# Optimization experiments

Measured on AMD Instinct MI355X. Metric: run time of the kernel, lower is better.

## Reference

```python
import jax, jax.numpy as jnp
import numpy as np

# --- static config (matches init_kwargs) ---
B, S, DIM = 1, 2048, 1024
H, G, DK, DV = 16, 4, 64, 64
HPG = H // G
L, D, LSEL, NSEL, W = 32, 16, 64, 16, 512
NCMP = (S - L) // D + 1            # number of compressed blocks over full prefill
J = S // LSEL                      # number of selection blocks
GH = 32                            # gate hidden
NEG = -1e30


def rope(x, pos):
    # x: [B, S, N, Dh]; llama-style half rotation
    Dh = x.shape[-1]
    inv = 1.0 / (10000.0 ** (np.arange(0, Dh, 2) / Dh))
    ang = pos[:, None] * inv[None, :]                      # [S, Dh/2]
    cos = jnp.asarray(np.cos(ang), jnp.float32)[None, :, None, :]
    sin = jnp.asarray(np.sin(ang), jnp.float32)[None, :, None, :]
    x1, x2 = jnp.split(x, 2, axis=-1)
    return jnp.concatenate([x1 * cos - x2 * sin, x2 * cos + x1 * sin], axis=-1)


def masked_softmax(s, m):
    p = jax.nn.softmax(jnp.where(m, s, NEG), axis=-1)
    # rows with no visible keys produce 0 output (empty attention)
    return jnp.where(jnp.any(m, axis=-1, keepdims=True), p, 0.0)


def setup_inputs() -> dict:
    key = jax.random.key(0)
    ks = jax.random.split(key, 12)
    def w(k, shape, fan):
        return jax.random.normal(k, shape, jnp.float32) / np.sqrt(fan)
    return {
        'x': jax.random.normal(ks[0], (B, S, DIM), jnp.float32),
        'W_Q': w(ks[1], (DIM, H * DK), DIM),
        'W_K_sel': w(ks[2], (DIM, G * DK), DIM),
        'W_V_sel': w(ks[3], (DIM, G * DV), DIM),
        'W_K_win': w(ks[4], (DIM, G * DK), DIM),
        'W_V_win': w(ks[5], (DIM, G * DV), DIM),
        'W_K_cmp': w(ks[6], (DIM, G * DK), DIM),
        'W_V_cmp': w(ks[7], (DIM, G * DV), DIM),
        'W_out': w(ks[8], (H * DV, DIM), H * DV),
        'gate_w1': w(ks[9], (DK, GH), DK),
        'gate_b1': jnp.zeros((GH,), jnp.float32),
        'gate_w2': 0.1 * jax.random.normal(ks[10], (GH, 3), jnp.float32),
        'gate_b2': jnp.zeros((3,), jnp.float32),
    }


def reference(x, W_Q, W_K_sel, W_V_sel, W_K_win, W_V_win, W_K_cmp, W_V_cmp,
              W_out, gate_w1, gate_b1, gate_w2, gate_b2):
    pos = np.arange(S)
    s_ = np.arange(S)
    scale = 1.0 / np.sqrt(DK)

    Q = rope((x @ W_Q).reshape(B, S, H, DK), pos).reshape(B, S, G, HPG, DK)

    def proj_kv(Wk, Wv):
        K = rope((x @ Wk).reshape(B, S, G, DK), pos).transpose(0, 2, 1, 3)  # [B,G,S,Dk]
        V = (x @ Wv).reshape(B, S, G, DV).transpose(0, 2, 1, 3)            # [B,G,S,Dv]
        return K, V

    K_sel, V_sel = proj_kv(W_K_sel, W_V_sel)
    K_win, V_win = proj_kv(W_K_win, W_V_win)
    K_cr, V_cr = proj_kv(W_K_cmp, W_V_cmp)

    # --- compressed branch: avg-pool (len L, stride D) of roped K / raw V ---
    bidx = np.arange(NCMP)[:, None] * D + np.arange(L)[None, :]   # [NCMP, L]
    K_cmp = K_cr[:, :, bidx].mean(axis=3)                         # [B,G,NCMP,Dk]
    V_cmp = V_cr[:, :, bidx].mean(axis=3)
    vis_c = (np.arange(NCMP)[None, :] * D + L) <= (s_[:, None] + 1)  # block fully in past
    sc_c = jnp.einsum('bsghd,bgcd->bsghc', Q, K_cmp) * scale
    p_cmp = masked_softmax(sc_c, jnp.asarray(vis_c)[None, :, None, None, :])
    O_cmp = jnp.einsum('bsghc,bgce->bsghe', p_cmp, V_cmp)

    # --- map compressed probs -> selection-block scores (overlap fractions) ---
    i0 = np.arange(NCMP)[:, None] * D
    j0 = np.arange(J)[None, :] * LSEL
    ov = np.maximum(0, np.minimum(i0 + L, j0 + LSEL) - np.maximum(i0, j0)) / L
    p_grp = jnp.einsum('bsghc,cj->bsgj', p_cmp, jnp.asarray(ov, np.float32))  # sum over heads in group

    vis_j = (np.arange(J)[None, :] * LSEL) <= s_[:, None]
    forced = (np.arange(J)[None, :] == 0) | (np.arange(J)[None, :] == (s_ // LSEL)[:, None])
    score = jnp.where(jnp.asarray(vis_j)[None, :, None, :], p_grp, NEG)
    score = jnp.where(jnp.asarray(forced)[None, :, None, :], 1e9, score)  # force block 0 + current block
    topj = jax.lax.top_k(score, NSEL)[1]                                   # [B,S,G,NSEL]
    blk = jax.nn.one_hot(topj, J, dtype=jnp.float32).sum(axis=-2) > 0      # [B,S,G,J]

    tok2blk = np.repeat(np.arange(J), LSEL)[:S]
    causal = s_[:, None] >= s_[None, :]                                    # u <= t
    sel_mask = blk[:, :, :, tok2blk] & jnp.asarray(causal)[None, :, None, :]  # [B,S,G,S]
    sc_s = jnp.einsum('bsghd,bgud->bsghu', Q, K_sel) * scale
    O_sel = jnp.einsum('bsghu,bgue->bsghe',
                       masked_softmax(sc_s, sel_mask[:, :, :, None, :]), V_sel)

    # --- sliding window branch ---
    win_mask = causal & (s_[None, :] > s_[:, None] - W)
    sc_w = jnp.einsum('bsghd,bgud->bsghu', Q, K_win) * scale
    O_win = jnp.einsum('bsghu,bgue->bsghe',
                       masked_softmax(sc_w, jnp.asarray(win_mask)[None, :, None, None, :]), V_win)

    # --- gating MLP on head-pooled query per group ---
    gl = jax.nn.silu(Q.mean(axis=3) @ gate_w1 + gate_b1) @ gate_w2 + gate_b2  # [B,S,G,3]
    pg = jax.nn.softmax(gl, axis=-1)
    t2 = jax.lax.top_k(gl, 2)[0]
    peaked = (t2[..., 0] - t2[..., 1]) > 50.0
    gates = jnp.where(peaked[..., None],
                      jax.nn.one_hot(jnp.argmax(gl, axis=-1), 3, dtype=gl.dtype), pg)

    O = (gates[..., 0, None, None] * O_cmp
         + gates[..., 1, None, None] * O_sel
         + gates[..., 2, None, None] * O_win)          # [B,S,G,h,Dv]
    return O.reshape(B, S, H * DV) @ W_out
```

## Files before the change

kernel.cpp:

```cpp
#include <hip/hip_runtime.h>
#include <math.h>

#define S 2048
#define DIM 1024
#define H 16
#define G 4
#define HPG 4
#define DK 64
#define DV 64
#define NCMP 127
#define JBLK 32
#define NSEL 16
#define WWIN 512
#define GH 32
#define SCL2 0.18033688011112042f

typedef __attribute__((ext_vector_type(8))) __bf16 bf16x8;
typedef __attribute__((ext_vector_type(4))) float f32x4;

__device__ __forceinline__ unsigned short f2bf(float f) {
  unsigned u = __float_as_uint(f);
  unsigned r = (u + 0x7FFFu + ((u >> 16) & 1u)) >> 16;
  return (unsigned short)r;
}

__device__ __forceinline__ unsigned short f2bf_hw(float f) {
  __bf16 b = (__bf16)f;
  return *(unsigned short*)&b;
}

__device__ __forceinline__ f32x4 mfma16(bf16x8 a, bf16x8 b, f32x4 c) {
  return __builtin_amdgcn_mfma_f32_16x16x32_bf16(a, b, c, 0, 0, 0);
}

__global__ void rope_table(float* __restrict__ cosT, float* __restrict__ sinT) {
  int idx = blockIdx.x * blockDim.x + threadIdx.x;
  if (idx >= S * 32) return;
  int s = idx >> 5, i = idx & 31;
  double inv = pow(10000.0, -2.0 * (double)i / 64.0);
  double ang = (double)s * inv;
  cosT[idx] = (float)cos(ang);
  sinT[idx] = (float)sin(ang);
}

__device__ __forceinline__ void gemm_body(const float* __restrict__ A,
                                          const float* __restrict__ B,
                                          float* __restrict__ C,
                                          int N, int K, int bm, int bn,
                                          float* As , float* Bs ) {
  int tid = threadIdx.x;
  int tr = tid >> 4, tc = tid & 15;
  float acc[4][4] = {{0.f}};
  int arow = tid >> 2;
  int kba = (tid & 3) << 3;
  int brow = tid >> 4;
  int bcol = (tid & 15) << 2;
  const float* Ab = A + (size_t)(bm * 64) * K;
  const float* Bb = B + bn * 64;

  float4 a0 = *(const float4*)(Ab + (size_t)arow * K + kba);
  float4 a1 = *(const float4*)(Ab + (size_t)arow * K + kba + 4);
  float4 b0 = *(const float4*)(Bb + (size_t)brow * N + bcol);
  float4 b1 = *(const float4*)(Bb + (size_t)(brow + 16) * N + bcol);

  for (int k0 = 0; k0 < K; k0 += 32) {
    __syncthreads();
    {
      float av[8] = {a0.x, a0.y, a0.z, a0.w, a1.x, a1.y, a1.z, a1.w};
#pragma unroll
      for (int i = 0; i < 8; ++i) {
        int k = kba + i;
        As[k * 64 + (arow ^ (((k >> 3) & 3) << 3))] = av[i];
      }
      *(float4*)&Bs[brow * 64 + bcol] = b0;
      *(float4*)&Bs[(brow + 16) * 64 + bcol] = b1;
    }
    __syncthreads();
    if (k0 + 32 < K) {
      a0 = *(const float4*)(Ab + (size_t)arow * K + k0 + 32 + kba);
      a1 = *(const float4*)(Ab + (size_t)arow * K + k0 + 32 + kba + 4);
      b0 = *(const float4*)(Bb + (size_t)(k0 + 32 + brow) * N + bcol);
      b1 = *(const float4*)(Bb + (size_t)(k0 + 32 + brow + 16) * N + bcol);
    }
#pragma unroll
    for (int kk = 0; kk < 32; ++kk) {
      float4 a = *(const float4*)&As[kk * 64 + ((tr << 2) ^ (((kk >> 3) & 3) << 3))];
      float4 b = *(const float4*)&Bs[kk * 64 + (tc << 2)];
      acc[0][0] += a.x * b.x; acc[0][1] += a.x * b.y; acc[0][2] += a.x * b.z; acc[0][3] += a.x * b.w;
      acc[1][0] += a.y * b.x; acc[1][1] += a.y * b.y; acc[1][2] += a.y * b.z; acc[1][3] += a.y * b.w;
      acc[2][0] += a.z * b.x; acc[2][1] += a.z * b.y; acc[2][2] += a.z * b.z; acc[2][3] += a.z * b.w;
      acc[3][0] += a.w * b.x; acc[3][1] += a.w * b.y; acc[3][2] += a.w * b.z; acc[3][3] += a.w * b.w;
    }
  }
  for (int i = 0; i < 4; ++i)
    for (int jj = 0; jj < 4; ++jj)
      C[(size_t)(bm * 64 + (tr << 2) + i) * N + bn * 64 + (tc << 2) + jj] = acc[i][jj];
}

__global__ __launch_bounds__(256) void gemm_f32(const float* __restrict__ A,
                                                const float* __restrict__ B,
                                                float* __restrict__ C,
                                                int N, int K) {
  __shared__ float As[32 * 64];
  __shared__ float Bs[32 * 64];
  gemm_body(A, B, C, N, K, blockIdx.y, blockIdx.x, As, Bs);
}

__global__ __launch_bounds__(256) void gemm_kv2(const float* __restrict__ x,
                                                const float* __restrict__ W0,
                                                const float* __restrict__ W1,
                                                float* __restrict__ out) {
  __shared__ float As[32 * 64];
  __shared__ float Bs[32 * 64];
  const float* B = blockIdx.z ? W1 : W0;
  gemm_body(x, B, out + (size_t)blockIdx.z * S * 256, 256, DIM, blockIdx.y,
            blockIdx.x, As, Bs);
}

__global__ void rope_apply(float* __restrict__ a, const float* __restrict__ cosT,
                           const float* __restrict__ sinT, int NH, int total) {
  int idx = blockIdx.x * blockDim.x + threadIdx.x;
  if (idx >= total) return;
  int i = idx & 31;
  int rest = idx >> 5;
  int n = rest % NH;
  int s = rest / NH;
  float c = cosT[s * 32 + i], sn = sinT[s * 32 + i];
  float* base = a + (size_t)(s * NH + n) * 64;
  float x1 = base[i], x2 = base[i + 32];
  base[i] = x1 * c - x2 * sn;
  base[i + 32] = x2 * c + x1 * sn;
}

__global__ __launch_bounds__(256) void fconv(const float* __restrict__ a,
                                             unsigned short* __restrict__ b) {
  int idx = (blockIdx.x * 256 + threadIdx.x) * 8;
  float4 x = *(const float4*)&a[idx];
  float4 y = *(const float4*)&a[idx + 4];
  union { unsigned short us[8]; float4 f4; } t;
  t.us[0] = f2bf(x.x); t.us[1] = f2bf(x.y); t.us[2] = f2bf(x.z); t.us[3] = f2bf(x.w);
  t.us[4] = f2bf(y.x); t.us[5] = f2bf(y.y); t.us[6] = f2bf(y.z); t.us[7] = f2bf(y.w);
  *(float4*)&b[idx] = t.f4;
}

__global__ __launch_bounds__(256) void wtrans(const float* __restrict__ W0,
                                              const float* __restrict__ W1,
                                              const float* __restrict__ W2,
                                              const float* __restrict__ W3,
                                              unsigned short* __restrict__ Wt) {
  __shared__ float t[64][65];
  int k0 = blockIdx.x * 64;
  int n0 = blockIdx.y * 64;
  int m = blockIdx.z;
  const float* W = (m == 0) ? W0 : (m == 1) ? W1 : (m == 2) ? W2 : W3;
  int tid = threadIdx.x;
  int rr = tid >> 4, c4 = (tid & 15) * 4;
#pragma unroll
  for (int e = 0; e < 4; ++e) {
    int row = rr + e * 16;
    float4 v = *(const float4*)(W + (size_t)(k0 + row) * 256 + n0 + c4);
    t[c4 + 0][row] = v.x;
    t[c4 + 1][row] = v.y;
    t[c4 + 2][row] = v.z;
    t[c4 + 3][row] = v.w;
  }
  __syncthreads();
#pragma unroll
  for (int e = 0; e < 2; ++e) {
    int flat = tid + e * 256;
    int col = flat >> 3, kc = (flat & 7) * 8;
    union { unsigned short us[8]; float4 f4; } u;
#pragma unroll
    for (int i = 0; i < 8; ++i) u.us[i] = f2bf(t[col][kc + i]);
    *(float4*)(Wt + ((size_t)m * 256 + n0 + col) * 1024 + k0 + kc) = u.f4;
  }
}

__global__ __launch_bounds__(256) void wtrans_o(const float* __restrict__ W,
                                                unsigned short* __restrict__ Wt) {
  __shared__ float t[64][65];
  int k0 = blockIdx.x * 64;
  int n0 = blockIdx.y * 64;
  int tid = threadIdx.x;
  int rr = tid >> 4, c4 = (tid & 15) * 4;
#pragma unroll
  for (int e = 0; e < 4; ++e) {
    int row = rr + e * 16;
    float4 v = *(const float4*)(W + (size_t)(k0 + row) * 1024 + n0 + c4);
    t[c4 + 0][row] = v.x;
    t[c4 + 1][row] = v.y;
    t[c4 + 2][row] = v.z;
    t[c4 + 3][row] = v.w;
  }
  __syncthreads();
#pragma unroll
  for (int e = 0; e < 2; ++e) {
    int flat = tid + e * 256;
    int col = flat >> 3, kc = (flat & 7) * 8;
    union { unsigned short us[8]; float4 f4; } u;
#pragma unroll
    for (int i = 0; i < 8; ++i) u.us[i] = f2bf(t[col][kc + i]);
    *(float4*)(Wt + (size_t)(n0 + col) * 1024 + k0 + kc) = u.f4;
  }
}

__global__ __launch_bounds__(256) void proj_bf16(
    const unsigned short* __restrict__ xb, const unsigned short* __restrict__ Wt,
    const float* __restrict__ cosT, const float* __restrict__ sinT,
    unsigned short* __restrict__ Kb_s, unsigned short* __restrict__ Vt_s,
    unsigned short* __restrict__ Kb_w, unsigned short* __restrict__ Vt_w) {
  __shared__ unsigned short xs[64 * 64];
  __shared__ unsigned short ws[64 * 64];
  int s0 = blockIdx.x * 64;
  int g = blockIdx.y;
  int mat = blockIdx.z;
  int tid = threadIdx.x, w = tid >> 6, lane = tid & 63;
  int l15 = lane & 15, lg = lane >> 4;
  int rswz = (l15 & 7) << 3;
  bool isV = (mat & 1);
  const unsigned short* wt = Wt + ((size_t)mat * 256 + g * 64) * 1024;

  f32x4 acc[4];
#pragma unroll
  for (int nt = 0; nt < 4; ++nt) acc[nt] = (f32x4){0.f, 0.f, 0.f, 0.f};

  for (int k0 = 0; k0 < DIM; k0 += 64) {
#pragma unroll
    for (int e = 0; e < 2; ++e) {
      int flat = tid + e * 256;
      int row = flat >> 3, cc = flat & 7;
      int dsti = row * 64 + ((cc ^ (row & 7)) << 3);
      *(float4*)&xs[dsti] = *(const float4*)(xb + (size_t)(s0 + row) * DIM + k0 + cc * 8);
      *(float4*)&ws[dsti] = *(const float4*)(wt + (size_t)row * DIM + k0 + cc * 8);
    }
    __syncthreads();
    const unsigned short* aP = isV ? ws : xs;
    const unsigned short* bP = isV ? xs : ws;
    int arow = w * 16 + l15;
    bf16x8 af[2];
#pragma unroll
    for (int kc = 0; kc < 2; ++kc)
      af[kc] = *(const bf16x8*)&aP[(arow * 64 + kc * 32 + lg * 8) ^ rswz];
#pragma unroll
    for (int nt = 0; nt < 4; ++nt) {
      int brow = nt * 16 + l15;
      bf16x8 b0 = *(const bf16x8*)&bP[(brow * 64 + lg * 8) ^ rswz];
      bf16x8 b1 = *(const bf16x8*)&bP[(brow * 64 + 32 + lg * 8) ^ rswz];
      acc[nt] = mfma16(af[0], b0, acc[nt]);
      acc[nt] = mfma16(af[1], b1, acc[nt]);
    }
    __syncthreads();
  }

  if (!isV) {
    unsigned short* Kb = (mat == 0) ? Kb_s : Kb_w;
#pragma unroll
    for (int rr = 0; rr < 4; ++rr) {
      int tok = s0 + w * 16 + lg * 4 + rr;
#pragma unroll
      for (int p = 0; p < 2; ++p) {
        int i = p * 16 + l15;
        float c = cosT[tok * 32 + i], sn = sinT[tok * 32 + i];
        float x1 = acc[p][rr], x2 = acc[p + 2][rr];
        Kb[((size_t)g * S + tok) * 64 + i] = f2bf(x1 * c - x2 * sn);
        Kb[((size_t)g * S + tok) * 64 + i + 32] = f2bf(x2 * c + x1 * sn);
      }
    }
  } else {
    unsigned short* Vt = (mat == 1) ? Vt_s : Vt_w;
#pragma unroll
    for (int rr = 0; rr < 4; ++rr) {
      int col = w * 16 + lg * 4 + rr;
#pragma unroll
      for (int nt = 0; nt < 4; ++nt) {
        int tok = s0 + nt * 16 + l15;
        Vt[((size_t)g * 64 + col) * S + tok] = f2bf(acc[nt][rr]);
      }
    }
  }
}

__global__ __launch_bounds__(256) void gemm_out(const unsigned short* __restrict__ Ob,
                                                const unsigned short* __restrict__ Wt,
                                                float* __restrict__ out) {
  __shared__ unsigned short xs[64 * 64];
  __shared__ unsigned short ws[64 * 64];
  int s0 = blockIdx.x * 64;
  int n0 = blockIdx.y * 64;
  int tid = threadIdx.x, w = tid >> 6, lane = tid & 63;
  int l15 = lane & 15, lg = lane >> 4;
  int rswz = (l15 & 7) << 3;

  f32x4 acc[4];
#pragma unroll
  for (int nt = 0; nt < 4; ++nt) acc[nt] = (f32x4){0.f, 0.f, 0.f, 0.f};

  for (int k0 = 0; k0 < DIM; k0 += 64) {
#pragma unroll
    for (int e = 0; e < 2; ++e) {
      int flat = tid + e * 256;
      int row = flat >> 3, cc = flat & 7;
      int dsti = row * 64 + ((cc ^ (row & 7)) << 3);
      *(float4*)&xs[dsti] = *(const float4*)(Ob + (size_t)(s0 + row) * DIM + k0 + cc * 8);
      *(float4*)&ws[dsti] = *(const float4*)(Wt + (size_t)(n0 + row) * DIM + k0 + cc * 8);
    }
    __syncthreads();
    int arow = w * 16 + l15;
    bf16x8 af0 = *(const bf16x8*)&xs[(arow * 64 + lg * 8) ^ rswz];
    bf16x8 af1 = *(const bf16x8*)&xs[(arow * 64 + 32 + lg * 8) ^ rswz];
#pragma unroll
    for (int nt = 0; nt < 4; ++nt) {
      int brow = nt * 16 + l15;
      bf16x8 b0 = *(const bf16x8*)&ws[(brow * 64 + lg * 8) ^ rswz];
      bf16x8 b1 = *(const bf16x8*)&ws[(brow * 64 + 32 + lg * 8) ^ rswz];
      acc[nt] = mfma16(af0, b0, acc[nt]);
      acc[nt] = mfma16(af1, b1, acc[nt]);
    }
    __syncthreads();
  }

#pragma unroll
  for (int nt = 0; nt < 4; ++nt)
#pragma unroll
    for (int rr = 0; rr < 4; ++rr)
      out[(size_t)(s0 + w * 16 + lg * 4 + rr) * 1024 + n0 + nt * 16 + l15] =
          acc[nt][rr];
}

__global__ void pool_cmp(const float* __restrict__ Kcr, const float* __restrict__ Vcr,
                         float* __restrict__ Kc, float* __restrict__ Vc) {
  int c = blockIdx.x, g = blockIdx.y, d = threadIdx.x;
  float sk = 0.f, sv = 0.f;
  for (int l = 0; l < 32; ++l) {
    int t = c * 16 + l;
    sk += Kcr[(size_t)(t * G + g) * 64 + d];
    sv += Vcr[(size_t)(t * G + g) * 64 + d];
  }
  Kc[(size_t)(g * NCMP + c) * 64 + d] = sk * (1.f / 32.f);
  Vc[(size_t)(g * NCMP + c) * 64 + d] = sv * (1.f / 32.f);
}

__global__ __launch_bounds__(256) void cmp_attn(const float* __restrict__ Q,
                                                const float* __restrict__ Kc,
                                                const float* __restrict__ Vc,
                                                float* __restrict__ Ocmp,
                                                unsigned int* __restrict__ selm) {
  int s = blockIdx.x, g = blockIdx.y;
  __shared__ float q4[4][64];
  __shared__ float sc[4][128];
  __shared__ float pg[JBLK];
  int tid = threadIdx.x;
  int nvis = (s >= 31) ? (((s - 31) >> 4) + 1) : 0;
  {
    int h = tid >> 6, d = tid & 63;
    q4[h][d] = Q[(size_t)(s * H + g * HPG + h) * 64 + d];
  }
  __syncthreads();

  if (tid < 128) {
    int c = tid;
    if (c < nvis) {
      float a0 = 0.f, a1 = 0.f, a2 = 0.f, a3 = 0.f;
      const float* kr = &Kc[(size_t)(g * NCMP + c) * 64];
#pragma unroll 4
      for (int kk = 0; kk < 16; ++kk) {
        float4 kv = *(const float4*)&kr[kk * 4];
        float4 q0 = *(const float4*)&q4[0][kk * 4];
        float4 q1 = *(const float4*)&q4[1][kk * 4];
        float4 q2 = *(const float4*)&q4[2][kk * 4];
        float4 q3 = *(const float4*)&q4[3][kk * 4];
        a0 += q0.x * kv.x + q0.y * kv.y + q0.z * kv.z + q0.w * kv.w;
        a1 += q1.x * kv.x + q1.y * kv.y + q1.z * kv.z + q1.w * kv.w;
        a2 += q2.x * kv.x + q2.y * kv.y + q2.z * kv.z + q2.w * kv.w;
        a3 += q3.x * kv.x + q3.y * kv.y + q3.z * kv.z + q3.w * kv.w;
      }
      sc[0][c] = a0 * 0.125f;
      sc[1][c] = a1 * 0.125f;
      sc[2][c] = a2 * 0.125f;
      sc[3][c] = a3 * 0.125f;
    } else {
      sc[0][c] = -INFINITY;
      sc[1][c] = -INFINITY;
      sc[2][c] = -INFINITY;
      sc[3][c] = -INFINITY;
    }
  }
  __syncthreads();

  int w = tid >> 6, lane = tid & 63;
  {
    float v0 = sc[w][lane];
    float v1 = (lane + 64 < NCMP) ? sc[w][lane + 64] : -INFINITY;
    float m = fmaxf(v0, v1);
    for (int off = 32; off; off >>= 1) m = fmaxf(m, __shfl_xor(m, off));
    float e0 = (m > -INFINITY && v0 > -INFINITY) ? expf(v0 - m) : 0.f;
    float e1 = (m > -INFINITY && v1 > -INFINITY) ? expf(v1 - m) : 0.f;
    float sum = e0 + e1;
    for (int off = 32; off; off >>= 1) sum += __shfl_xor(sum, off);
    float inv = (sum > 0.f) ? 1.f / sum : 0.f;
    sc[w][lane] = e0 * inv;
    if (lane + 64 < NCMP) sc[w][lane + 64] = e1 * inv;
    if (lane == 63) sc[w][127] = 0.f;
  }
  __syncthreads();

  {
    int h = tid >> 6, d = tid & 63;
    float o = 0.f;
#pragma unroll 4
    for (int c = 0; c < nvis; ++c) o += sc[h][c] * Vc[(size_t)(g * NCMP + c) * 64 + d];
    Ocmp[(size_t)(s * H + g * HPG + h) * 64 + d] = o;
  }

  if (tid < JBLK) {
    int j = tid;
    float a = 0.f;
#pragma unroll
    for (int h = 0; h < 4; ++h) {
      const float* row = sc[h];
      float v = row[4 * j] + row[4 * j + 1] + row[4 * j + 2] + 0.5f * row[4 * j + 3];
      if (j > 0) v += 0.5f * row[4 * j - 1];
      a += v;
    }
    pg[j] = a;
  }
  __syncthreads();

  if (tid < 64) {
    int j = tid & 31;
    int cur = s >> 6;
    float v = (j * 64 <= s) ? pg[j] : -1e30f;
    if (j == 0 || j == cur) v = 1e9f;
    unsigned int mask = 0;
#pragma unroll 1
    for (int n = 0; n < NSEL; ++n) {
      float bv = v;
      int bj = j;
#pragma unroll
      for (int off = 1; off < 32; off <<= 1) {
        float ov = __shfl_xor(bv, off);
        int oj = __shfl_xor(bj, off);
        if (ov > bv || (ov == bv && oj < bj)) { bv = ov; bj = oj; }
      }
      mask |= 1u << bj;
      if (j == bj) v = -INFINITY;
    }
    if (tid == 0) selm[(size_t)s * G + g] = mask;
  }
}

__global__ __launch_bounds__(256) void attn_fused(
    const unsigned short* __restrict__ Qbf,
    const unsigned short* __restrict__ Kbs, const unsigned short* __restrict__ Vts,
    const unsigned short* __restrict__ Kbw, const unsigned short* __restrict__ Vtw,
    const unsigned int* __restrict__ selm,
    float* __restrict__ Osel, float* __restrict__ Owin) {
  __shared__ unsigned short Kl[64 * 64];
  __shared__ unsigned short Vt[64 * 64];
  __shared__ unsigned short Pl[4][16 * 64];
  __shared__ unsigned int sel_l[16];
  __shared__ int blist[JBLK];
  __shared__ int nB_s;

  int t0 = blockIdx.x * 16;
  int g = blockIdx.y;
  int mode = blockIdx.z;
  int tid = threadIdx.x;
  int w = tid >> 6, lane = tid & 63;
  int l15 = lane & 15, lg = lane >> 4;
  int rswz = (l15 & 7) << 3;
  int jdiag = t0 >> 6;

  const unsigned short* Kb = mode ? Kbw : Kbs;
  const unsigned short* Vtb = mode ? Vtw : Vts;
  float* O = mode ? Owin : Osel;

  if (mode == 0 && tid < 16) sel_l[tid] = selm[(t0 + tid) * G + g];
  __syncthreads();
  if (tid == 0) {
    int n = 0;
    if (mode == 0) {
      unsigned int un = 0;
      for (int i = 0; i < 16; ++i) un |= sel_l[i];
      for (int j = 0; j <= jdiag; ++j)
        if ((un >> j) & 1u) blist[n++] = j;
    } else {
      int lo = t0 - (WWIN - 1);
      int j0 = (lo > 0) ? (lo >> 6) : 0;
      for (int j = j0; j <= jdiag; ++j) blist[n++] = j;
    }
    nB_s = n;
  }
  __syncthreads();
  int nB = nB_s;

  int tok = t0 + l15;
  bf16x8 qf[2];
  {
    const unsigned short* qb = Qbf + ((size_t)tok * H + g * HPG + w) * 64;
    qf[0] = *(const bf16x8*)(qb + lg * 8);
    qf[1] = *(const bf16x8*)(qb + 32 + lg * 8);
  }

  float mrun = -INFINITY, lrun = 0.f;
  f32x4 oacc[4];
#pragma unroll
  for (int dt = 0; dt < 4; ++dt) oacc[dt] = (f32x4){0.f, 0.f, 0.f, 0.f};

  for (int b = 0; b < nB; ++b) {
    int j = blist[b];
    int ku = j * 64;

    {
      const unsigned short* src = Kb + ((size_t)g * S + ku) * 64;
#pragma unroll
      for (int c2 = 0; c2 < 2; ++c2) {
        int chunk = tid + c2 * 256;
        int key = chunk >> 3, cc = chunk & 7;
        *(float4*)&Kl[key * 64 + ((cc ^ (key & 7)) << 3)] =
            *(const float4*)(src + chunk * 8);
      }
#pragma unroll
      for (int c2 = 0; c2 < 2; ++c2) {
        int chunk = tid + c2 * 256;
        int dim = chunk >> 3, cc = chunk & 7;
        *(float4*)&Vt[dim * 64 + ((cc ^ (dim & 7)) << 3)] =
            *(const float4*)(Vtb + ((size_t)g * 64 + dim) * S + ku + cc * 8);
      }
    }
    __syncthreads();

    f32x4 sf[4];
#pragma unroll
    for (int kt = 0; kt < 4; ++kt) sf[kt] = (f32x4){0.f, 0.f, 0.f, 0.f};
#pragma unroll
    for (int kt = 0; kt < 4; ++kt) {
      int krow = kt * 16 + l15;
      bf16x8 kf0 = *(const bf16x8*)&Kl[(krow * 64 + lg * 8) ^ rswz];
      bf16x8 kf1 = *(const bf16x8*)&Kl[(krow * 64 + 32 + lg * 8) ^ rswz];
      sf[kt] = mfma16(kf0, qf[0], sf[kt]);
      sf[kt] = mfma16(kf1, qf[1], sf[kt]);
    }

    bool bsel = true;
    if (mode == 0) bsel = ((sel_l[l15] >> j) & 1u) != 0;
    float sv2[4][4];
    if (j == jdiag) {
#pragma unroll
      for (int kt = 0; kt < 4; ++kt)
#pragma unroll
        for (int rr = 0; rr < 4; ++rr) {
          int u = ku + kt * 16 + lg * 4 + rr;
          sv2[kt][rr] = (u <= tok) ? sf[kt][rr] * SCL2 : -INFINITY;
        }
    } else if (mode == 1 && (ku + WWIN <= t0 + 15)) {
#pragma unroll
      for (int kt = 0; kt < 4; ++kt)
#pragma unroll
        for (int rr = 0; rr < 4; ++rr) {
          int u = ku + kt * 16 + lg * 4 + rr;
          sv2[kt][rr] = (u + WWIN > tok) ? sf[kt][rr] * SCL2 : -INFINITY;
        }
    } else {
#pragma unroll
      for (int kt = 0; kt < 4; ++kt)
#pragma unroll
        for (int rr = 0; rr < 4; ++rr) sv2[kt][rr] = sf[kt][rr] * SCL2;
    }

    float pmax = -INFINITY;
#pragma unroll
    for (int kt = 0; kt < 4; ++kt)
#pragma unroll
      for (int rr = 0; rr < 4; ++rr) pmax = fmaxf(pmax, sv2[kt][rr]);
    pmax = fmaxf(pmax, __shfl_xor(pmax, 16));
    pmax = fmaxf(pmax, __shfl_xor(pmax, 32));
    if (mode == 0 && !bsel) pmax = -INFINITY;

    if (__any(pmax > mrun)) {
      float mnew = fmaxf(mrun, pmax);
      float mc = (mnew == -INFINITY) ? 0.f : mnew;
      float fac = exp2f(mrun - mc);
      mrun = mnew;
      lrun *= fac;
#pragma unroll
      for (int dt = 0; dt < 4; ++dt)
#pragma unroll
        for (int rr = 0; rr < 4; ++rr) oacc[dt][rr] *= fac;
    }
    float mcb = (mode == 0 && !bsel) ? INFINITY
                                     : ((mrun == -INFINITY) ? 0.f : mrun);

    float psum = 0.f;
    unsigned short pb[16];
#pragma unroll
    for (int kt = 0; kt < 4; ++kt)
#pragma unroll
      for (int rr = 0; rr < 4; ++rr) {
        float e = exp2f(sv2[kt][rr] - mcb);
        psum += e;
        pb[kt * 4 + rr] = f2bf_hw(e);
      }
    psum += __shfl_xor(psum, 16);
    psum += __shfl_xor(psum, 32);
    lrun += psum;

    {
      unsigned short* pw = &Pl[w][0];
#pragma unroll
      for (int kt = 0; kt < 4; ++kt) {
        int idx = (l15 * 64 + kt * 16 + lg * 4) ^ rswz;
        unsigned int lo = (unsigned)pb[kt * 4] | ((unsigned)pb[kt * 4 + 1] << 16);
        unsigned int hi = (unsigned)pb[kt * 4 + 2] | ((unsigned)pb[kt * 4 + 3] << 16);
        *(uint2*)&pw[idx] = make_uint2(lo, hi);
      }
    }

#pragma unroll
    for (int kc = 0; kc < 2; ++kc) {
      bf16x8 pf = *(const bf16x8*)&Pl[w][(l15 * 64 + kc * 32 + lg * 8) ^ rswz];
#pragma unroll
      for (int dt = 0; dt < 4; ++dt) {
        bf16x8 vf = *(const bf16x8*)&Vt[((dt * 16 + l15) * 64 + kc * 32 + lg * 8) ^ rswz];
        oacc[dt] = mfma16(vf, pf, oacc[dt]);
      }
    }
    __syncthreads();
  }

  {
    float inv = (lrun > 0.f) ? 1.f / lrun : 0.f;
    float* ob = O + ((size_t)tok * H + g * HPG + w) * 64;
#pragma unroll
    for (int dt = 0; dt < 4; ++dt) {
      float4 v;
      v.x = oacc[dt][0] * inv;
      v.y = oacc[dt][1] * inv;
      v.z = oacc[dt][2] * inv;
      v.w = oacc[dt][3] * inv;
      *(float4*)(ob + dt * 16 + lg * 4) = v;
    }
  }
}

__global__ void gate_kernel(const float* __restrict__ Q, const float* __restrict__ w1,
                            const float* __restrict__ b1, const float* __restrict__ w2,
                            const float* __restrict__ b2, float* __restrict__ gates) {
  int idx = blockIdx.x * blockDim.x + threadIdx.x;
  if (idx >= S * G) return;
  int s = idx >> 2, g = idx & 3;
  float qm[64];
#pragma unroll
  for (int d = 0; d < 64; ++d) {
    float a = 0.f;
    for (int hp = 0; hp < HPG; ++hp) a += Q[(size_t)(s * H + g * HPG + hp) * 64 + d];
    qm[d] = a * 0.25f;
  }
  float gl[3] = {b2[0], b2[1], b2[2]};
  for (int j = 0; j < GH; ++j) {
    float z = b1[j];
    for (int d = 0; d < 64; ++d) z += qm[d] * w1[d * GH + j];
    float sl = z / (1.f + expf(-z));
    gl[0] += sl * w2[j * 3 + 0];
    gl[1] += sl * w2[j * 3 + 1];
    gl[2] += sl * w2[j * 3 + 2];
  }
  float m = fmaxf(gl[0], fmaxf(gl[1], gl[2]));
  float e0 = expf(gl[0] - m), e1 = expf(gl[1] - m), e2 = expf(gl[2] - m);
  float inv = 1.f / (e0 + e1 + e2);
  float p0 = e0 * inv, p1 = e1 * inv, p2 = e2 * inv;
  int am = (gl[0] >= gl[1] && gl[0] >= gl[2]) ? 0 : ((gl[1] >= gl[2]) ? 1 : 2);
  float t1 = (am == 0) ? fmaxf(gl[1], gl[2]) : ((am == 1) ? fmaxf(gl[0], gl[2]) : fmaxf(gl[0], gl[1]));
  if (m - t1 > 50.f) {
    p0 = (am == 0) ? 1.f : 0.f;
    p1 = (am == 1) ? 1.f : 0.f;
    p2 = (am == 2) ? 1.f : 0.f;
  }
  gates[idx * 3 + 0] = p0;
  gates[idx * 3 + 1] = p1;
  gates[idx * 3 + 2] = p2;
}

__global__ void combine(const float* __restrict__ Oc, const float* __restrict__ Os,
                        const float* __restrict__ Ow, const float* __restrict__ gates,
                        unsigned short* __restrict__ Ob) {
  int idx = blockIdx.x * blockDim.x + threadIdx.x;
  if (idx >= S * H * DV) return;
  int h = (idx >> 6) & 15;
  int s = idx >> 10;
  int g = h >> 2;
  const float* gp = &gates[(size_t)(s * G + g) * 3];
  Ob[idx] = f2bf(gp[0] * Oc[idx] + gp[1] * Os[idx] + gp[2] * Ow[idx]);
}

extern "C" void kernel_launch(void* const* d_in, const int* in_sizes, int n_in,
                              void* d_out, int out_size, void* d_ws, size_t ws_size,
                              hipStream_t stream) {
  const float* x = (const float*)d_in[0];
  const float* W_Q = (const float*)d_in[1];
  const float* W_K_sel = (const float*)d_in[2];
  const float* W_V_sel = (const float*)d_in[3];
  const float* W_K_win = (const float*)d_in[4];
  const float* W_V_win = (const float*)d_in[5];
  const float* W_K_cmp = (const float*)d_in[6];
  const float* W_V_cmp = (const float*)d_in[7];
  const float* W_out = (const float*)d_in[8];
  const float* gw1 = (const float*)d_in[9];
  const float* gb1 = (const float*)d_in[10];
  const float* gw2 = (const float*)d_in[11];
  const float* gb2 = (const float*)d_in[12];

  float* w = (float*)d_ws;
  float* cosT = w;  w += S * 32;
  float* sinT = w;  w += S * 32;
  float* Qb   = w;  w += S * H * DK;
  float* Kcr  = w;  w += S * G * DK;
  float* Vcr  = w;  w += S * G * DV;
  float* Kc   = w;  w += G * NCMP * DK;
  float* Vc   = w;  w += G * NCMP * DV;
  float* Ocmp = w;  w += S * H * DV;
  float* Osel = w;  w += S * H * DV;
  float* Owin = w;  w += S * H * DV;
  float* gates= w;  w += S * G * 3;
  unsigned int* selm = (unsigned int*)w;  w += S * G;
  unsigned short* Kbf_s = (unsigned short*)w;  w += (size_t)G * S * 64 / 2;
  unsigned short* Kbf_w = (unsigned short*)w;  w += (size_t)G * S * 64 / 2;
  unsigned short* Vt_s  = (unsigned short*)w;  w += (size_t)G * S * 64 / 2;
  unsigned short* Vt_w  = (unsigned short*)w;  w += (size_t)G * S * 64 / 2;
  unsigned short* Qbf   = (unsigned short*)w;  w += (size_t)S * H * 64 / 2;
  unsigned short* xb    = (unsigned short*)w;  w += (size_t)S * DIM / 2;
  unsigned short* Wt    = (unsigned short*)w;  w += (size_t)4 * 256 * DIM / 2;
  unsigned short* Ob    = (unsigned short*)w;  w += (size_t)S * H * DV / 2;
  unsigned short* WtO   = (unsigned short*)w;  w += (size_t)DIM * DIM / 2;

  rope_table<<<(S * 32 + 255) / 256, 256, 0, stream>>>(cosT, sinT);
  fconv<<<(S * DIM) / 2048, 256, 0, stream>>>(x, xb);
  wtrans<<<dim3(DIM / 64, 4, 4), 256, 0, stream>>>(W_K_sel, W_V_sel, W_K_win,
                                                   W_V_win, Wt);
  wtrans_o<<<dim3(DIM / 64, DIM / 64), 256, 0, stream>>>(W_out, WtO);

  gemm_f32<<<dim3(DIM / 64, S / 64), 256, 0, stream>>>(x, W_Q, Qb, H * DK, DIM);
  gemm_kv2<<<dim3(4, S / 64, 2), 256, 0, stream>>>(x, W_K_cmp, W_V_cmp, Kcr);

  rope_apply<<<(S * H * 32 + 255) / 256, 256, 0, stream>>>(Qb, cosT, sinT, H, S * H * 32);
  rope_apply<<<(S * G * 32 + 255) / 256, 256, 0, stream>>>(Kcr, cosT, sinT, G, S * G * 32);

  proj_bf16<<<dim3(S / 64, G, 4), 256, 0, stream>>>(xb, Wt, cosT, sinT, Kbf_s, Vt_s,
                                                    Kbf_w, Vt_w);
  fconv<<<(S * H * 64) / 2048, 256, 0, stream>>>(Qb, Qbf);

  pool_cmp<<<dim3(NCMP, G), 64, 0, stream>>>(Kcr, Vcr, Kc, Vc);

  cmp_attn<<<dim3(S, G), 256, 0, stream>>>(Qb, Kc, Vc, Ocmp, selm);
  attn_fused<<<dim3(S / 16, G, 2), 256, 0, stream>>>(Qbf, Kbf_s, Vt_s, Kbf_w, Vt_w,
                                                     selm, Osel, Owin);

  gate_kernel<<<(S * G + 255) / 256, 256, 0, stream>>>(Qb, gw1, gb1, gw2, gb2, gates);
  combine<<<(S * H * DV + 255) / 256, 256, 0, stream>>>(Ocmp, Osel, Owin, gates, Ob);

  gemm_out<<<dim3(S / 64, DIM / 64), 256, 0, stream>>>(Ob, WtO, (float*)d_out);
}
```

Before: 339.9 us.

## Split-K fused Q/Kcmp fp32 GEMM, fuse rope+bf16 conversion, move V_cmp to bf16 MFMA

```diff
diff --git a/kernel.cpp b/kernel.cpp
--- a/kernel.cpp
+++ b/kernel.cpp
@@ -29,6 +29,10 @@
   return *(unsigned short*)&b;
 }
 
+__device__ __forceinline__ float bf2f(unsigned short u) {
+  return __uint_as_float((unsigned)u << 16);
+}
+
 __device__ __forceinline__ f32x4 mfma16(bf16x8 a, bf16x8 b, f32x4 c) {
   return __builtin_amdgcn_mfma_f32_16x16x32_bf16(a, b, c, 0, 0, 0);
 }
@@ -43,11 +47,12 @@
   sinT[idx] = (float)sin(ang);
 }
 
-__device__ __forceinline__ void gemm_body(const float* __restrict__ A,
-                                          const float* __restrict__ B,
-                                          float* __restrict__ C,
-                                          int N, int K, int bm, int bn,
-                                          float* As , float* Bs ) {
+__device__ __forceinline__ void gemm_body_k(const float* __restrict__ A,
+                                            const float* __restrict__ B,
+                                            float* __restrict__ C,
+                                            int N, int K, int bm, int bn,
+                                            int kS, int kE,
+                                            float* As, float* Bs) {
   int tid = threadIdx.x;
   int tr = tid >> 4, tc = tid & 15;
   float acc[4][4] = {{0.f}};
@@ -58,12 +63,12 @@
   const float* Ab = A + (size_t)(bm * 64) * K;
   const float* Bb = B + bn * 64;
 
-  float4 a0 = *(const float4*)(Ab + (size_t)arow * K + kba);
-  float4 a1 = *(const float4*)(Ab + (size_t)arow * K + kba + 4);
-  float4 b0 = *(const float4*)(Bb + (size_t)brow * N + bcol);
-  float4 b1 = *(const float4*)(Bb + (size_t)(brow + 16) * N + bcol);
-
-  for (int k0 = 0; k0 < K; k0 += 32) {
+  float4 a0 = *(const float4*)(Ab + (size_t)arow * K + kS + kba);
+  float4 a1 = *(const float4*)(Ab + (size_t)arow * K + kS + kba + 4);
+  float4 b0 = *(const float4*)(Bb + (size_t)(kS + brow) * N + bcol);
+  float4 b1 = *(const float4*)(Bb + (size_t)(kS + brow + 16) * N + bcol);
+
+  for (int k0 = kS; k0 < kE; k0 += 32) {
     __syncthreads();
     {
       float av[8] = {a0.x, a0.y, a0.z, a0.w, a1.x, a1.y, a1.z, a1.w};
@@ -76,7 +81,7 @@
       *(float4*)&Bs[(brow + 16) * 64 + bcol] = b1;
     }
     __syncthreads();
-    if (k0 + 32 < K) {
+    if (k0 + 32 < kE) {
       a0 = *(const float4*)(Ab + (size_t)arow * K + k0 + 32 + kba);
       a1 = *(const float4*)(Ab + (size_t)arow * K + k0 + 32 + kba + 4);
       b0 = *(const float4*)(Bb + (size_t)(k0 + 32 + brow) * N + bcol);
@@ -97,39 +102,56 @@
       C[(size_t)(bm * 64 + (tr << 2) + i) * N + bn * 64 + (tc << 2) + jj] = acc[i][jj];
 }
 
-__global__ __launch_bounds__(256) void gemm_f32(const float* __restrict__ A,
-                                                const float* __restrict__ B,
-                                                float* __restrict__ C,
-                                                int N, int K) {
+__global__ __launch_bounds__(256) void gemm_qk(const float* __restrict__ x,
+                                               const float* __restrict__ W_Q,
+                                               const float* __restrict__ W_Kc,
+                                               float* __restrict__ Pq,
+                                               float* __restrict__ Pk) {
   __shared__ float As[32 * 64];
   __shared__ float Bs[32 * 64];
-  gemm_body(A, B, C, N, K, blockIdx.y, blockIdx.x, As, Bs);
-}
-
-__global__ __launch_bounds__(256) void gemm_kv2(const float* __restrict__ x,
-                                                const float* __restrict__ W0,
-                                                const float* __restrict__ W1,
-                                                float* __restrict__ out) {
-  __shared__ float As[32 * 64];
-  __shared__ float Bs[32 * 64];
-  const float* B = blockIdx.z ? W1 : W0;
-  gemm_body(x, B, out + (size_t)blockIdx.z * S * 256, 256, DIM, blockIdx.y,
-            blockIdx.x, As, Bs);
-}
-
-__global__ void rope_apply(float* __restrict__ a, const float* __restrict__ cosT,
-                           const float* __restrict__ sinT, int NH, int total) {
-  int idx = blockIdx.x * blockDim.x + threadIdx.x;
-  if (idx >= total) return;
-  int i = idx & 31;
-  int rest = idx >> 5;
-  int n = rest % NH;
-  int s = rest / NH;
-  float c = cosT[s * 32 + i], sn = sinT[s * 32 + i];
-  float* base = a + (size_t)(s * NH + n) * 64;
-  float x1 = base[i], x2 = base[i + 32];
-  base[i] = x1 * c - x2 * sn;
-  base[i + 32] = x2 * c + x1 * sn;
+  int ct = blockIdx.x, bm = blockIdx.y, z = blockIdx.z;
+  int kS = z * 512, kE = kS + 512;
+  if (ct < 16)
+    gemm_body_k(x, W_Q, Pq + (size_t)z * S * 1024, 1024, DIM, bm, ct, kS, kE, As, Bs);
+  else
+    gemm_body_k(x, W_Kc, Pk + (size_t)z * S * 256, 256, DIM, bm, ct - 16, kS, kE, As, Bs);
+}
+
+__global__ __launch_bounds__(256) void reduce_rope(
+    const float* __restrict__ Pq, const float* __restrict__ Pk,
+    const float* __restrict__ cosT, const float* __restrict__ sinT,
+    float* __restrict__ Qb, unsigned short* __restrict__ Qbf,
+    float* __restrict__ Kcr) {
+  int idx = blockIdx.x * 256 + threadIdx.x;
+  const int NQ = S * H * 32;
+  if (idx < NQ) {
+    int i = idx & 31;
+    int rest = idx >> 5;
+    int h = rest & 15;
+    int s = rest >> 4;
+    size_t base = (size_t)s * 1024 + h * 64 + i;
+    float a1 = Pq[base] + Pq[(size_t)S * 1024 + base];
+    float a2 = Pq[base + 32] + Pq[(size_t)S * 1024 + base + 32];
+    float c = cosT[s * 32 + i], sn = sinT[s * 32 + i];
+    float q1 = a1 * c - a2 * sn, q2 = a2 * c + a1 * sn;
+    Qb[base] = q1;
+    Qb[base + 32] = q2;
+    Qbf[base] = f2bf(q1);
+    Qbf[base + 32] = f2bf(q2);
+  } else {
+    int j = idx - NQ;
+    if (j >= S * G * 32) return;
+    int i = j & 31;
+    int rest = j >> 5;
+    int g = rest & 3;
+    int s = rest >> 2;
+    size_t base = (size_t)s * 256 + g * 64 + i;
+    float a1 = Pk[base] + Pk[(size_t)S * 256 + base];
+    float a2 = Pk[base + 32] + Pk[(size_t)S * 256 + base + 32];
+    float c = cosT[s * 32 + i], sn = sinT[s * 32 + i];
+    Kcr[base] = a1 * c - a2 * sn;
+    Kcr[base + 32] = a2 * c + a1 * sn;
+  }
 }
 
 __global__ __launch_bounds__(256) void fconv(const float* __restrict__ a,
@@ -147,12 +169,13 @@
                                               const float* __restrict__ W1,
                                               const float* __restrict__ W2,
                                               const float* __restrict__ W3,
+                                              const float* __restrict__ W4,
                                               unsigned short* __restrict__ Wt) {
   __shared__ float t[64][65];
   int k0 = blockIdx.x * 64;
   int n0 = blockIdx.y * 64;
   int m = blockIdx.z;
-  const float* W = (m == 0) ? W0 : (m == 1) ? W1 : (m == 2) ? W2 : W3;
+  const float* W = (m == 0) ? W0 : (m == 1) ? W1 : (m == 2) ? W2 : (m == 3) ? W3 : W4;
   int tid = threadIdx.x;
   int rr = tid >> 4, c4 = (tid & 15) * 4;
 #pragma unroll
@@ -208,7 +231,8 @@
     const unsigned short* __restrict__ xb, const unsigned short* __restrict__ Wt,
     const float* __restrict__ cosT, const float* __restrict__ sinT,
     unsigned short* __restrict__ Kb_s, unsigned short* __restrict__ Vt_s,
-    unsigned short* __restrict__ Kb_w, unsigned short* __restrict__ Vt_w) {
+    unsigned short* __restrict__ Kb_w, unsigned short* __restrict__ Vt_w,
+    unsigned short* __restrict__ Vt_c) {
   __shared__ unsigned short xs[64 * 64];
   __shared__ unsigned short ws[64 * 64];
   int s0 = blockIdx.x * 64;
@@ -217,7 +241,7 @@
   int tid = threadIdx.x, w = tid >> 6, lane = tid & 63;
   int l15 = lane & 15, lg = lane >> 4;
   int rswz = (l15 & 7) << 3;
-  bool isV = (mat & 1);
+  bool isV = (mat == 1) || (mat == 3) || (mat == 4);
   const unsigned short* wt = Wt + ((size_t)mat * 256 + g * 64) * 1024;
 
   f32x4 acc[4];
@@ -267,7 +291,7 @@
       }
     }
   } else {
-    unsigned short* Vt = (mat == 1) ? Vt_s : Vt_w;
+    unsigned short* Vt = (mat == 1) ? Vt_s : (mat == 3) ? Vt_w : Vt_c;
 #pragma unroll
     for (int rr = 0; rr < 4; ++rr) {
       int col = w * 16 + lg * 4 + rr;
@@ -327,14 +351,15 @@
           acc[nt][rr];
 }
 
-__global__ void pool_cmp(const float* __restrict__ Kcr, const float* __restrict__ Vcr,
+__global__ void pool_cmp(const float* __restrict__ Kcr,
+                         const unsigned short* __restrict__ Vtc,
                          float* __restrict__ Kc, float* __restrict__ Vc) {
   int c = blockIdx.x, g = blockIdx.y, d = threadIdx.x;
   float sk = 0.f, sv = 0.f;
+  const unsigned short* vrow = Vtc + ((size_t)g * 64 + d) * S + c * 16;
   for (int l = 0; l < 32; ++l) {
-    int t = c * 16 + l;
-    sk += Kcr[(size_t)(t * G + g) * 64 + d];
-    sv += Vcr[(size_t)(t * G + g) * 64 + d];
+    sk += Kcr[(size_t)((c * 16 + l) * G + g) * 64 + d];
+    sv += bf2f(vrow[l]);
   }
   Kc[(size_t)(g * NCMP + c) * 64 + d] = sk * (1.f / 32.f);
   Vc[(size_t)(g * NCMP + c) * 64 + d] = sv * (1.f / 32.f);
@@ -715,7 +740,6 @@
   float* sinT = w;  w += S * 32;
   float* Qb   = w;  w += S * H * DK;
   float* Kcr  = w;  w += S * G * DK;
-  float* Vcr  = w;  w += S * G * DV;
   float* Kc   = w;  w += G * NCMP * DK;
   float* Vc   = w;  w += G * NCMP * DV;
   float* Ocmp = w;  w += S * H * DV;
@@ -727,29 +751,30 @@
   unsigned short* Kbf_w = (unsigned short*)w;  w += (size_t)G * S * 64 / 2;
   unsigned short* Vt_s  = (unsigned short*)w;  w += (size_t)G * S * 64 / 2;
   unsigned short* Vt_w  = (unsigned short*)w;  w += (size_t)G * S * 64 / 2;
+  unsigned short* Vt_c  = (unsigned short*)w;  w += (size_t)G * S * 64 / 2;
   unsigned short* Qbf   = (unsigned short*)w;  w += (size_t)S * H * 64 / 2;
   unsigned short* xb    = (unsigned short*)w;  w += (size_t)S * DIM / 2;
-  unsigned short* Wt    = (unsigned short*)w;  w += (size_t)4 * 256 * DIM / 2;
+  unsigned short* Wt    = (unsigned short*)w;  w += (size_t)5 * 256 * DIM / 2;
   unsigned short* Ob    = (unsigned short*)w;  w += (size_t)S * H * DV / 2;
   unsigned short* WtO   = (unsigned short*)w;  w += (size_t)DIM * DIM / 2;
 
+  float* Pq = Ocmp;
+  float* Pk = Owin;
+
   rope_table<<<(S * 32 + 255) / 256, 256, 0, stream>>>(cosT, sinT);
   fconv<<<(S * DIM) / 2048, 256, 0, stream>>>(x, xb);
-  wtrans<<<dim3(DIM / 64, 4, 4), 256, 0, stream>>>(W_K_sel, W_V_sel, W_K_win,
-                                                   W_V_win, Wt);
+  wtrans<<<dim3(DIM / 64, 4, 5), 256, 0, stream>>>(W_K_sel, W_V_sel, W_K_win,
+                                                   W_V_win, W_V_cmp, Wt);
   wtrans_o<<<dim3(DIM / 64, DIM / 64), 256, 0, stream>>>(W_out, WtO);
 
-  gemm_f32<<<dim3(DIM / 64, S / 64), 256, 0, stream>>>(x, W_Q, Qb, H * DK, DIM);
-  gemm_kv2<<<dim3(4, S / 64, 2), 256, 0, stream>>>(x, W_K_cmp, W_V_cmp, Kcr);
-
-  rope_apply<<<(S * H * 32 + 255) / 256, 256, 0, stream>>>(Qb, cosT, sinT, H, S * H * 32);
-  rope_apply<<<(S * G * 32 + 255) / 256, 256, 0, stream>>>(Kcr, cosT, sinT, G, S * G * 32);
-
-  proj_bf16<<<dim3(S / 64, G, 4), 256, 0, stream>>>(xb, Wt, cosT, sinT, Kbf_s, Vt_s,
-                                                    Kbf_w, Vt_w);
-  fconv<<<(S * H * 64) / 2048, 256, 0, stream>>>(Qb, Qbf);
-
-  pool_cmp<<<dim3(NCMP, G), 64, 0, stream>>>(Kcr, Vcr, Kc, Vc);
+  gemm_qk<<<dim3(20, S / 64, 2), 256, 0, stream>>>(x, W_Q, W_K_cmp, Pq, Pk);
+  reduce_rope<<<(S * (H + G) * 32) / 256, 256, 0, stream>>>(Pq, Pk, cosT, sinT,
+                                                            Qb, Qbf, Kcr);
+
+  proj_bf16<<<dim3(S / 64, G, 5), 256, 0, stream>>>(xb, Wt, cosT, sinT, Kbf_s, Vt_s,
+                                                    Kbf_w, Vt_w, Vt_c);
+
+  pool_cmp<<<dim3(NCMP, G), 64, 0, stream>>>(Kcr, Vt_c, Kc, Vc);
 
   cmp_attn<<<dim3(S, G), 256, 0, stream>>>(Qb, Kc, Vc, Ocmp, selm);
   attn_fused<<<dim3(S / 16, G, 2), 256, 0, stream>>>(Qbf, Kbf_s, Vt_s, Kbf_w, Vt_w,
```

Measured after the change: 307.1 us. -9.6%, faster.
